# Optimization experiments

Measured on AMD Instinct MI355X. Metric: run time of the kernel, lower is better.

Reference implementation:

```python
import jax, jax.numpy as jnp
import numpy as np

N_NODES = 50000
N_EDGES = 800000
IN_FEATS = 256
HIDDEN = 128
HEADS = 2
NEG_SLOPE = 0.2


def gat_conv(x, edge_index, W, att_src, att_dst, bias, heads, out_c, concat):
    """PyG-style GATConv: linear -> per-edge attention logits -> segment
    softmax over destination neighborhoods -> scatter-add aggregate.
    Self-loops are added (PyG default add_self_loops=True)."""
    N = x.shape[0]
    h = (x @ W.T).reshape(N, heads, out_c)           # [N,H,C]
    loop = jnp.arange(N)
    src = jnp.concatenate([edge_index[0], loop])      # [E+N]
    dst = jnp.concatenate([edge_index[1], loop])
    a_src = jnp.sum(h * att_src, axis=-1)             # [N,H]
    a_dst = jnp.sum(h * att_dst, axis=-1)
    alpha = a_src[src] + a_dst[dst]                   # [E+N,H]
    alpha = jax.nn.leaky_relu(alpha, NEG_SLOPE)
    amax = jax.ops.segment_max(alpha, dst, num_segments=N)
    alpha = jnp.exp(alpha - amax[dst])
    denom = jax.ops.segment_sum(alpha, dst, num_segments=N)
    alpha = alpha / denom[dst]
    msg = h[src] * alpha[..., None]                   # [E+N,H,C]
    out = jax.ops.segment_sum(msg, dst, num_segments=N)  # [N,H,C]
    if concat:
        out = out.reshape(N, heads * out_c)
    else:
        out = out.mean(axis=1)
    return out + bias


def setup_inputs() -> dict:
    key = jax.random.key(0)
    ks = jax.random.split(key, 12)
    x = jax.random.normal(ks[0], (N_NODES, IN_FEATS), dtype=jnp.float32)
    edge_index = jax.random.randint(ks[1], (2, N_EDGES), 0, N_NODES, dtype=jnp.int64)
    s = 0.1
    W1 = jax.random.normal(ks[2], (HEADS * HIDDEN, IN_FEATS), dtype=jnp.float32) * s
    att_src1 = jax.random.normal(ks[3], (1, HEADS, HIDDEN), dtype=jnp.float32) * s
    att_dst1 = jax.random.normal(ks[4], (1, HEADS, HIDDEN), dtype=jnp.float32) * s
    b1 = jnp.zeros((HEADS * HIDDEN,), dtype=jnp.float32)
    W2 = jax.random.normal(ks[5], (HIDDEN, HEADS * HIDDEN), dtype=jnp.float32) * s
    att_src2 = jax.random.normal(ks[6], (1, 1, HIDDEN), dtype=jnp.float32) * s
    att_dst2 = jax.random.normal(ks[7], (1, 1, HIDDEN), dtype=jnp.float32) * s
    b2 = jnp.zeros((HIDDEN,), dtype=jnp.float32)
    return {"x": x, "edge_index": edge_index,
            "W1": W1, "att_src1": att_src1, "att_dst1": att_dst1, "b1": b1,
            "W2": W2, "att_src2": att_src2, "att_dst2": att_dst2, "b2": b2}


def reference(x, edge_index, W1, att_src1, att_dst1, b1, W2, att_src2, att_dst2, b2):
    h = gat_conv(x, edge_index, W1, att_src1, att_dst1, b1, HEADS, HIDDEN, True)
    h = jax.nn.relu(h)
    out = gat_conv(h, edge_index, W2, att_src2, att_dst2, b2, 1, HIDDEN, False)
    return out
```

## Files before the change

### kernel.cpp

```cpp
#include <hip/hip_runtime.h>
#include <hip/hip_bf16.h>


typedef _Float16 half8v __attribute__((ext_vector_type(8)));
typedef _Float16 half4v __attribute__((ext_vector_type(4)));
typedef _Float16 half2v __attribute__((ext_vector_type(2)));
typedef float f32x4 __attribute__((ext_vector_type(4)));


template <typename TA, int H, bool SCATTER>
__global__ __launch_bounds__(256) void gemm_att_kernel(
    const TA* __restrict__ A,
    const float* __restrict__ B,
    _Float16* __restrict__ C,
    const float* __restrict__ att_s,
    const float* __restrict__ att_d,
    float* __restrict__ a_s,
    float* __restrict__ a_d,
    int M, int K, int GB,
    const int* __restrict__ esrc, const int* __restrict__ edst,
    const int* __restrict__ rank, const int* __restrict__ csr_off,
    int* __restrict__ csr_src, int E, int nScatBlk)
{
    constexpr int BM = 128, BK = 32, LDA = 40;
    constexpr int NCOL = H * 128;
    __shared__ _Float16 Ah[BM * LDA];
    __shared__ _Float16 Bh[BM * LDA];
    __shared__ float red[2][2][64][2];

    const int tid = threadIdx.x;
    const int bid = blockIdx.x;

    if constexpr (SCATTER) {
        if (bid >= GB * H) {
            const int sbid = bid - GB * H;
            const int nq = (E + 3) >> 2;
            for (int q = sbid * 256 + tid; q < nq; q += nScatBlk * 256) {
                const int e4 = q * 4;
                if (e4 + 3 < E) {
                    const int4 sv = *reinterpret_cast<const int4*>(esrc + e4);
                    const int4 dv = *reinterpret_cast<const int4*>(edst + e4);
                    const int4 rv = *reinterpret_cast<const int4*>(rank + e4);
                    csr_src[csr_off[dv.x] + 1 + rv.x] = sv.x;
                    csr_src[csr_off[dv.y] + 1 + rv.y] = sv.y;
                    csr_src[csr_off[dv.z] + 1 + rv.z] = sv.z;
                    csr_src[csr_off[dv.w] + 1 + rv.w] = sv.w;
                } else {
                    for (int k = e4; k < E; ++k)
                        csr_src[csr_off[edst[k]] + 1 + rank[k]] = esrc[k];
                }
            }
            return;
        }
    }

    const int m0 = (bid % GB) * BM;
    const int by = bid / GB;
    const int n0 = by * 128;
    const int w  = tid >> 6;
    const int l  = tid & 63;
    const int wm = (w >> 1) * 64;
    const int wn = (w & 1) * 64;
    const int lr = l & 15;
    const int lq = l >> 4;

    f32x4 acc[4][4] = {};

    for (int k0 = 0; k0 < K; k0 += BK) {
        if constexpr (__is_same(TA, float)) {
#pragma unroll
            for (int it = 0; it < 4; ++it) {
                const int row = (tid >> 3) + it * 32;
                const int gm  = min(m0 + row, M - 1);
                const int c4  = (tid & 7) * 4;
                float4 v = *reinterpret_cast<const float4*>(A + (long)gm * K + k0 + c4);
                half4v o = { (_Float16)v.x, (_Float16)v.y, (_Float16)v.z, (_Float16)v.w };
                *reinterpret_cast<half4v*>(&Ah[row * LDA + c4]) = o;
            }
        } else {
#pragma unroll
            for (int it = 0; it < 2; ++it) {
                const int row = (tid >> 2) + it * 64;
                const int gm  = min(m0 + row, M - 1);
                const int c8  = (tid & 3) * 8;
                float4 v = *reinterpret_cast<const float4*>((const char*)A + ((long)gm * K + k0 + c8) * 2);
                *reinterpret_cast<float4*>(&Ah[row * LDA + c8]) = v;
            }
        }
#pragma unroll
        for (int it = 0; it < 4; ++it) {
            const int row = (tid >> 3) + it * 32;
            const int c4  = (tid & 7) * 4;
            float4 v = *reinterpret_cast<const float4*>(B + (long)(n0 + row) * K + k0 + c4);
            half4v o = { (_Float16)v.x, (_Float16)v.y, (_Float16)v.z, (_Float16)v.w };
            *reinterpret_cast<half4v*>(&Bh[row * LDA + c4]) = o;
        }
        __syncthreads();

        half8v af[4], bf[4];
#pragma unroll
        for (int i = 0; i < 4; ++i)
            af[i] = *reinterpret_cast<const half8v*>(&Ah[(wm + i * 16 + lr) * LDA + lq * 8]);
#pragma unroll
        for (int j = 0; j < 4; ++j)
            bf[j] = *reinterpret_cast<const half8v*>(&Bh[(wn + j * 16 + lr) * LDA + lq * 8]);
#pragma unroll
        for (int i = 0; i < 4; ++i)
#pragma unroll
            for (int j = 0; j < 4; ++j)
                acc[i][j] = __builtin_amdgcn_mfma_f32_16x16x32_f16(af[i], bf[j], acc[i][j], 0, 0, 0);
        __syncthreads();
    }

#pragma unroll
    for (int i = 0; i < 4; ++i) {
        const int gm_base = m0 + wm + i * 16 + lq * 4;
#pragma unroll
        for (int r = 0; r < 4; ++r) {
            const int gm = gm_base + r;
            if (gm < M) {
#pragma unroll
                for (int j = 0; j < 4; ++j)
                    C[(long)gm * NCOL + n0 + wn + j * 16 + lr] = (_Float16)acc[i][j][r];
            }
        }
    }

    float asv[4], adv[4];
#pragma unroll
    for (int j = 0; j < 4; ++j) {
        asv[j] = att_s[n0 + wn + j * 16 + lr];
        adv[j] = att_d[n0 + wn + j * 16 + lr];
    }
    float ps[4][4] = {}, pd[4][4] = {};
#pragma unroll
    for (int i = 0; i < 4; ++i)
#pragma unroll
        for (int j = 0; j < 4; ++j)
#pragma unroll
            for (int r = 0; r < 4; ++r) {
                ps[i][r] += acc[i][j][r] * asv[j];
                pd[i][r] += acc[i][j][r] * adv[j];
            }
#pragma unroll
    for (int o = 1; o < 16; o <<= 1)
#pragma unroll
        for (int i = 0; i < 4; ++i)
#pragma unroll
            for (int r = 0; r < 4; ++r) {
                ps[i][r] += __shfl_xor(ps[i][r], o, 64);
                pd[i][r] += __shfl_xor(pd[i][r], o, 64);
            }
    if (lr == 0) {
#pragma unroll
        for (int i = 0; i < 4; ++i)
#pragma unroll
            for (int r = 0; r < 4; ++r) {
                const int row = i * 16 + lq * 4 + r;
                red[wm >> 6][wn >> 6][row][0] = ps[i][r];
                red[wm >> 6][wn >> 6][row][1] = pd[i][r];
            }
    }
    __syncthreads();
    if (wn == 0) {
        const int row = l;
        const int gm = m0 + wm + row;
        if (gm < M) {
            const int wi = wm >> 6;
            a_s[(long)gm * H + by] = red[wi][0][row][0] + red[wi][1][row][0];
            a_d[(long)gm * H + by] = red[wi][0][row][1] + red[wi][1][row][1];
        }
    }
}


__global__ void count_kernel(const int* __restrict__ dst, int* __restrict__ deg,
                             int* __restrict__ rank, int E)
{
    const int tid = blockIdx.x * blockDim.x + threadIdx.x;
    const int e4 = tid * 4;
    if (e4 + 3 < E) {
        const int4 d = *reinterpret_cast<const int4*>(dst + e4);
        int4 r;
        r.x = atomicAdd(&deg[d.x], 1);
        r.y = atomicAdd(&deg[d.y], 1);
        r.z = atomicAdd(&deg[d.z], 1);
        r.w = atomicAdd(&deg[d.w], 1);
        *reinterpret_cast<int4*>(rank + e4) = r;
    } else if (e4 < E) {
        for (int k = e4; k < E; ++k) rank[k] = atomicAdd(&deg[dst[k]], 1);
    }
}

__global__ __launch_bounds__(256) void block_scan_kernel(
    const int* __restrict__ deg, int* __restrict__ pre, int* __restrict__ blk, int n)
{
    __shared__ int s[256];
    const int t = threadIdx.x;
    const int base = blockIdx.x * 1024 + t * 4;
    int4 d = make_int4(-1, -1, -1, -1);
    if (base + 3 < n) d = *reinterpret_cast<const int4*>(deg + base);
    else {
        if (base + 0 < n) d.x = deg[base + 0];
        if (base + 1 < n) d.y = deg[base + 1];
        if (base + 2 < n) d.z = deg[base + 2];
        if (base + 3 < n) d.w = deg[base + 3];
    }
    const int v0 = d.x + 1, v1 = d.y + 1, v2 = d.z + 1, v3 = d.w + 1;
    s[t] = v0 + v1 + v2 + v3;
    __syncthreads();
#pragma unroll
    for (int o = 1; o < 256; o <<= 1) {
        int val = 0;
        if (t >= o) val = s[t - o];
        __syncthreads();
        s[t] += val;
        __syncthreads();
    }
    int run = (t == 0) ? 0 : s[t - 1];
    int4 o4;
    o4.x = run; run += v0;
    o4.y = run; run += v1;
    o4.z = run; run += v2;
    o4.w = run; run += v3;
    if (base + 3 < n) *reinterpret_cast<int4*>(pre + base) = o4;
    else {
        if (base + 0 < n) pre[base + 0] = o4.x;
        if (base + 1 < n) pre[base + 1] = o4.y;
        if (base + 2 < n) pre[base + 2] = o4.z;
        if (base + 3 < n) pre[base + 3] = o4.w;
    }
    if (t == 255) blk[blockIdx.x] = s[255];
}

__global__ __launch_bounds__(256) void finalize_scan_kernel(
    const int* __restrict__ pre, const int* __restrict__ blk,
    int* __restrict__ off, int* __restrict__ csr_src, int n, int nvb)
{
    __shared__ int s_add;
    const int vb = blockIdx.x;
    const int t  = threadIdx.x;
    if (t < 64) {
        int v = (t < vb) ? blk[t] : 0;
#pragma unroll
        for (int o = 32; o > 0; o >>= 1) v += __shfl_xor(v, o, 64);
        if (t == 0) s_add = v;
    }
    __syncthreads();
    const int add = s_add;
    const int base = vb * 1024 + t * 4;
    if (base + 3 < n) {
        int4 p = *reinterpret_cast<const int4*>(pre + base);
        p.x += add; p.y += add; p.z += add; p.w += add;
        *reinterpret_cast<int4*>(off + base) = p;
        csr_src[p.x] = base + 0;
        csr_src[p.y] = base + 1;
        csr_src[p.z] = base + 2;
        csr_src[p.w] = base + 3;
    } else {
#pragma unroll
        for (int k = 0; k < 4; ++k)
            if (base + k < n) {
                const int v = pre[base + k] + add;
                off[base + k] = v;
                csr_src[v] = base + k;
            }
    }
    if (vb == nvb - 1 && t == 0) off[n] = add + blk[vb];
}


template <int H, int C, bool RELU, typename TOUT>
__global__ __launch_bounds__(256) void aggregate_kernel(
    const int* __restrict__ csr_off,
    const int* __restrict__ csr_src,
    const _Float16* __restrict__ h,
    const float* __restrict__ a_s,
    const float* __restrict__ a_d,
    const float* __restrict__ bias,
    TOUT* __restrict__ out,
    int N)
{
    constexpr int VPT = 8;
    constexpr int HC  = H * C;
    constexpr int LPE = HC / VPT;
    constexpr int GRP = 64 / LPE;

    const int w = threadIdx.x >> 6;
    const int l = threadIdx.x & 63;
    const int d = blockIdx.x * 4 + w;
    if (d >= N) return;

    const int g   = l / LPE;
    const int col = (l % LPE) * VPT;
    const int hh  = col / C;

    __shared__ float2 s_sw[4][64][H];

    const int beg = csr_off[d];
    const int end = csr_off[d + 1];

    float ad0 = 0.f, ad1 = 0.f;
    if constexpr (H == 2) {
        const float2 t2 = *reinterpret_cast<const float2*>(a_d + (long)d * 2);
        ad0 = t2.x; ad1 = t2.y;
    } else {
        ad0 = a_d[d];
    }

    float acc[VPT] = {};
    float wsum = 0.f;

    for (int base = beg; base < end; base += 64) {
        const int len  = min(64, end - base);
        const int lenp = (len + GRP - 1) & ~(GRP - 1);
        if (l < len) {
            const int s = csr_src[base + l];
            if constexpr (H == 2) {
                const float2 sv = *reinterpret_cast<const float2*>(a_s + (long)s * 2);
                float lg0 = sv.x + ad0; lg0 = lg0 > 0.f ? lg0 : 0.2f * lg0;
                float lg1 = sv.y + ad1; lg1 = lg1 > 0.f ? lg1 : 0.2f * lg1;
                s_sw[w][l][0] = make_float2(__int_as_float(s), __expf(lg0));
                s_sw[w][l][1] = make_float2(__int_as_float(s), __expf(lg1));
            } else {
                float lg = a_s[s] + ad0; lg = lg > 0.f ? lg : 0.2f * lg;
                s_sw[w][l][0] = make_float2(__int_as_float(s), __expf(lg));
            }
        } else if (l < lenp) {
#pragma unroll
            for (int h2 = 0; h2 < H; ++h2)
                s_sw[w][l][h2] = make_float2(__int_as_float(d), 0.f);
        }
        __builtin_amdgcn_wave_barrier();
#pragma unroll 2
        for (int jj = 0; jj < lenp; jj += GRP) {
            const float2 sw = s_sw[w][jj + g][hh];
            const int    s  = __float_as_int(sw.x);
            const float  wt = sw.y;
            const half8v hv = *reinterpret_cast<const half8v*>(
                h + (long)s * HC + col);
#pragma unroll
            for (int k = 0; k < VPT; ++k)
                acc[k] += wt * (float)hv[k];
            wsum += wt;
        }
        __builtin_amdgcn_wave_barrier();
    }

#pragma unroll
    for (int o = LPE; o < 64; o <<= 1) {
#pragma unroll
        for (int k = 0; k < VPT; ++k) acc[k] += __shfl_xor(acc[k], o, 64);
        wsum += __shfl_xor(wsum, o, 64);
    }

    if (g == 0) {
        const float inv = 1.f / wsum;
        float r[VPT];
#pragma unroll
        for (int k = 0; k < VPT; ++k) {
            r[k] = acc[k] * inv + bias[col + k];
            if (RELU) r[k] = r[k] > 0.f ? r[k] : 0.f;
        }
        if constexpr (__is_same(TOUT, _Float16)) {
            half8v ov;
#pragma unroll
            for (int k = 0; k < VPT; ++k) ov[k] = (_Float16)r[k];
            *reinterpret_cast<half8v*>(out + (long)d * HC + col) = ov;
        } else {
            f32x4 o0 = { r[0], r[1], r[2], r[3] };
            f32x4 o1 = { r[4], r[5], r[6], r[7] };
            *reinterpret_cast<f32x4*>(out + (long)d * HC + col)     = o0;
            *reinterpret_cast<f32x4*>(out + (long)d * HC + col + 4) = o1;
        }
    }
}


extern "C" void kernel_launch(void* const* d_in, const int* in_sizes, int n_in,
                              void* d_out, int out_size, void* d_ws, size_t ws_size,
                              hipStream_t stream)
{
    const float* x    = (const float*)d_in[0];
    const int*   eidx = (const int*)d_in[1];
    const float* W1   = (const float*)d_in[2];
    const float* as1  = (const float*)d_in[3];
    const float* ad1  = (const float*)d_in[4];
    const float* b1   = (const float*)d_in[5];
    const float* W2   = (const float*)d_in[6];
    const float* as2  = (const float*)d_in[7];
    const float* ad2  = (const float*)d_in[8];
    const float* b2   = (const float*)d_in[9];
    float* out = (float*)d_out;

    const int IN_FEATS = 256;
    const int N = in_sizes[0] / IN_FEATS;
    const int E = in_sizes[1] / 2;

    const int* esrc = eidx;
    const int* edst = eidx + E;

    size_t off = 0;
    auto alloc = [&](size_t bytes) -> void* {
        void* p = (char*)d_ws + off;
        off += (bytes + 255) & ~(size_t)255;
        return p;
    };
    _Float16* h1h   = (_Float16*)alloc((size_t)N * 256 * 2);
    _Float16* o1h   = (_Float16*)alloc((size_t)N * 256 * 2);
    _Float16* h2h   = (_Float16*)alloc((size_t)N * 128 * 2);
    float* a1s      = (float*)alloc((size_t)N * 2 * 4);
    float* a1d      = (float*)alloc((size_t)N * 2 * 4);
    float* a2s      = (float*)alloc((size_t)N * 4);
    float* a2d      = (float*)alloc((size_t)N * 4);
    int*   deg      = (int*)alloc((size_t)N * 4);
    int*   pre      = (int*)alloc((size_t)N * 4);
    int*   rank     = (int*)alloc((size_t)E * 4);
    int*   csr_off  = (int*)alloc((size_t)(N + 1) * 4);
    int*   csr_src  = (int*)alloc((size_t)(E + N) * 4);
    int*   blk      = (int*)alloc(64 * 4);

    const int nvb = (N + 1023) / 1024;

    hipMemsetAsync(deg, 0, (size_t)N * 4, stream);
    count_kernel<<<((E + 3) / 4 + 255) / 256, 256, 0, stream>>>(edst, deg, rank, E);
    block_scan_kernel<<<nvb, 256, 0, stream>>>(deg, pre, blk, N);
    finalize_scan_kernel<<<nvb, 256, 0, stream>>>(pre, blk, csr_off, csr_src, N, nvb);

    {
        const int GB = (N + 127) / 128;
        const int nScat = 192;
        gemm_att_kernel<float, 2, true><<<GB * 2 + nScat, 256, 0, stream>>>(
            x, W1, h1h, as1, ad1, a1s, a1d, N, 256, GB,
            esrc, edst, rank, csr_off, csr_src, E, nScat);
    }
    aggregate_kernel<2, 128, true, _Float16><<<(N + 3) / 4, 256, 0, stream>>>(
        csr_off, csr_src, h1h, a1s, a1d, b1, o1h, N);

    {
        const int GB = (N + 127) / 128;
        gemm_att_kernel<_Float16, 1, false><<<GB, 256, 0, stream>>>(
            o1h, W2, h2h, as2, ad2, a2s, a2d, N, 256, GB,
            nullptr, nullptr, nullptr, nullptr, nullptr, 0, 0);
    }
    aggregate_kernel<1, 128, false, float><<<(N + 3) / 4, 256, 0, stream>>>(
        csr_off, csr_src, h2h, a2s, a2d, b2, out, N);
}
```

Measured before the change: 292.7 us.

## Store features in 32-column sliced layout and aggregate per slice for cache locality

The GEMM outputs and first-layer aggregate outputs now use a column-sliced layout (32 fp16 columns per slice, each slice stored contiguously over all nodes). The aggregation kernel becomes persistent and grid-strided, and each block handles one slice, so the gathered working set per slice is small enough to stay in L2/LLC. Block-to-tile mapping in the first GEMM is swizzled so the two column halves of neighbouring row tiles run together. The cost is redundant re-reading of CSR indices and attention logits for every slice (eight times for layer one), plus narrower 8-byte gathers.

```diff
diff --git a/kernel.cpp b/kernel.cpp
--- a/kernel.cpp
+++ b/kernel.cpp
@@ -54,8 +54,15 @@
         }
     }
 
-    const int m0 = (bid % GB) * BM;
-    const int by = bid / GB;
+    int m0, by;
+    if (H == 2 && (GB & 7) == 0) {
+        const int cc = bid >> 4, jj = bid & 15;
+        m0 = ((cc << 3) + (jj & 7)) * BM;
+        by = jj >> 3;
+    } else {
+        m0 = (bid % GB) * BM;
+        by = bid / GB;
+    }
     const int n0 = by * 128;
     const int w  = tid >> 6;
     const int l  = tid & 63;
@@ -83,7 +90,9 @@
                 const int row = (tid >> 2) + it * 64;
                 const int gm  = min(m0 + row, M - 1);
                 const int c8  = (tid & 3) * 8;
-                float4 v = *reinterpret_cast<const float4*>((const char*)A + ((long)gm * K + k0 + c8) * 2);
+                const _Float16* src = (const _Float16*)A +
+                    ((size_t)(k0 >> 5) * M + gm) * 32 + c8;
+                float4 v = *reinterpret_cast<const float4*>(src);
                 *reinterpret_cast<float4*>(&Ah[row * LDA + c8]) = v;
             }
         }
@@ -120,8 +129,11 @@
             const int gm = gm_base + r;
             if (gm < M) {
 #pragma unroll
-                for (int j = 0; j < 4; ++j)
-                    C[(long)gm * NCOL + n0 + wn + j * 16 + lr] = (_Float16)acc[i][j][r];
+                for (int j = 0; j < 4; ++j) {
+                    const int col = n0 + wn + j * 16 + lr;
+                    C[((size_t)(col >> 5) * M + gm) * 32 + (col & 31)] =
+                        (_Float16)acc[i][j][r];
+                }
             }
         }
     }
@@ -279,99 +291,85 @@
     const float* __restrict__ a_d,
     const float* __restrict__ bias,
     TOUT* __restrict__ out,
-    int N)
-{
-    constexpr int VPT = 8;
+    int N, int G8)
+{
     constexpr int HC  = H * C;
-    constexpr int LPE = HC / VPT;
-    constexpr int GRP = 64 / LPE;
-
-    const int w = threadIdx.x >> 6;
-    const int l = threadIdx.x & 63;
-    const int d = blockIdx.x * 4 + w;
-    if (d >= N) return;
-
-    const int g   = l / LPE;
-    const int col = (l % LPE) * VPT;
-    const int hh  = col / C;
-
-    __shared__ float2 s_sw[4][64][H];
-
-    const int beg = csr_off[d];
-    const int end = csr_off[d + 1];
-
-    float ad0 = 0.f, ad1 = 0.f;
-    if constexpr (H == 2) {
-        const float2 t2 = *reinterpret_cast<const float2*>(a_d + (long)d * 2);
-        ad0 = t2.x; ad1 = t2.y;
-    } else {
-        ad0 = a_d[d];
-    }
-
-    float acc[VPT] = {};
-    float wsum = 0.f;
-
-    for (int base = beg; base < end; base += 64) {
-        const int len  = min(64, end - base);
-        const int lenp = (len + GRP - 1) & ~(GRP - 1);
-        if (l < len) {
-            const int s = csr_src[base + l];
-            if constexpr (H == 2) {
-                const float2 sv = *reinterpret_cast<const float2*>(a_s + (long)s * 2);
-                float lg0 = sv.x + ad0; lg0 = lg0 > 0.f ? lg0 : 0.2f * lg0;
-                float lg1 = sv.y + ad1; lg1 = lg1 > 0.f ? lg1 : 0.2f * lg1;
-                s_sw[w][l][0] = make_float2(__int_as_float(s), __expf(lg0));
-                s_sw[w][l][1] = make_float2(__int_as_float(s), __expf(lg1));
+    constexpr int NS  = HC / 32;
+    constexpr int REP = 8 / NS;
+    const int w  = threadIdx.x >> 6;
+    const int l  = threadIdx.x & 63;
+    const int b8 = blockIdx.x & 7;
+    const int slice = b8 % NS;
+    const int hh = (slice * 32) / C;
+    const int g2 = (blockIdx.x >> 3) * REP + b8 / NS;
+    const int dstride = G8 * REP * 4;
+    const int g  = l >> 3;
+    const int cl = (l & 7) * 4;
+
+    __shared__ float2 s_sw[4][64];
+    const _Float16* __restrict__ hs = h + (size_t)slice * N * 32;
+
+    for (int d = g2 * 4 + w; d < N; d += dstride) {
+        const int beg = csr_off[d];
+        const int end = csr_off[d + 1];
+        const float ad = a_d[d * H + hh];
+        float acc[4] = {};
+        float wsum = 0.f;
+
+        for (int base = beg; base < end; base += 64) {
+            const int len = min(64, end - base);
+            float2 sw;
+            if (l < len) {
+                const int s = __builtin_nontemporal_load(csr_src + base + l);
+                float lg = a_s[s * H + hh] + ad;
+                lg = lg > 0.f ? lg : 0.2f * lg;
+                sw = make_float2(__int_as_float(s), __expf(lg));
             } else {
-                float lg = a_s[s] + ad0; lg = lg > 0.f ? lg : 0.2f * lg;
-                s_sw[w][l][0] = make_float2(__int_as_float(s), __expf(lg));
-            }
-        } else if (l < lenp) {
-#pragma unroll
-            for (int h2 = 0; h2 < H; ++h2)
-                s_sw[w][l][h2] = make_float2(__int_as_float(d), 0.f);
-        }
-        __builtin_amdgcn_wave_barrier();
-#pragma unroll 2
-        for (int jj = 0; jj < lenp; jj += GRP) {
-            const float2 sw = s_sw[w][jj + g][hh];
-            const int    s  = __float_as_int(sw.x);
-            const float  wt = sw.y;
-            const half8v hv = *reinterpret_cast<const half8v*>(
-                h + (long)s * HC + col);
-#pragma unroll
-            for (int k = 0; k < VPT; ++k)
-                acc[k] += wt * (float)hv[k];
-            wsum += wt;
-        }
-        __builtin_amdgcn_wave_barrier();
-    }
-
-#pragma unroll
-    for (int o = LPE; o < 64; o <<= 1) {
-#pragma unroll
-        for (int k = 0; k < VPT; ++k) acc[k] += __shfl_xor(acc[k], o, 64);
-        wsum += __shfl_xor(wsum, o, 64);
-    }
-
-    if (g == 0) {
-        const float inv = 1.f / wsum;
-        float r[VPT];
-#pragma unroll
-        for (int k = 0; k < VPT; ++k) {
-            r[k] = acc[k] * inv + bias[col + k];
-            if (RELU) r[k] = r[k] > 0.f ? r[k] : 0.f;
-        }
-        if constexpr (__is_same(TOUT, _Float16)) {
-            half8v ov;
-#pragma unroll
-            for (int k = 0; k < VPT; ++k) ov[k] = (_Float16)r[k];
-            *reinterpret_cast<half8v*>(out + (long)d * HC + col) = ov;
-        } else {
-            f32x4 o0 = { r[0], r[1], r[2], r[3] };
-            f32x4 o1 = { r[4], r[5], r[6], r[7] };
-            *reinterpret_cast<f32x4*>(out + (long)d * HC + col)     = o0;
-            *reinterpret_cast<f32x4*>(out + (long)d * HC + col + 4) = o1;
+                sw = make_float2(__int_as_float(d), 0.f);
+            }
+            s_sw[w][l] = sw;
+            __builtin_amdgcn_wave_barrier();
+            const int iters = (len + 7) >> 3;
+            for (int jj = 0; jj < iters; ++jj) {
+                const float2 e = s_sw[w][jj * 8 + g];
+                const int    s = __float_as_int(e.x);
+                const float wt = e.y;
+                const half4v hv = *reinterpret_cast<const half4v*>(
+                    hs + (size_t)s * 32 + cl);
+                acc[0] += wt * (float)hv.x;
+                acc[1] += wt * (float)hv.y;
+                acc[2] += wt * (float)hv.z;
+                acc[3] += wt * (float)hv.w;
+                wsum += wt;
+            }
+            __builtin_amdgcn_wave_barrier();
+        }
+
+#pragma unroll
+        for (int o = 8; o < 64; o <<= 1) {
+#pragma unroll
+            for (int k = 0; k < 4; ++k) acc[k] += __shfl_xor(acc[k], o, 64);
+            wsum += __shfl_xor(wsum, o, 64);
+        }
+
+        if (g == 0) {
+            const float inv = 1.f / wsum;
+            float r[4];
+#pragma unroll
+            for (int k = 0; k < 4; ++k) {
+                r[k] = acc[k] * inv + bias[slice * 32 + cl + k];
+                if (RELU) r[k] = r[k] > 0.f ? r[k] : 0.f;
+            }
+            if constexpr (__is_same(TOUT, _Float16)) {
+                half4v ov = { (_Float16)r[0], (_Float16)r[1],
+                              (_Float16)r[2], (_Float16)r[3] };
+                *reinterpret_cast<half4v*>(
+                    out + ((size_t)slice * N + d) * 32 + cl) = ov;
+            } else {
+                f32x4 ov = { r[0], r[1], r[2], r[3] };
+                *reinterpret_cast<f32x4*>(
+                    out + (size_t)d * HC + slice * 32 + cl) = ov;
+            }
         }
     }
 }
@@ -434,8 +432,11 @@
             x, W1, h1h, as1, ad1, a1s, a1d, N, 256, GB,
             esrc, edst, rank, csr_off, csr_src, E, nScat);
     }
-    aggregate_kernel<2, 128, true, _Float16><<<(N + 3) / 4, 256, 0, stream>>>(
-        csr_off, csr_src, h1h, a1s, a1d, b1, o1h, N);
+    {
+        const int G8 = 256;
+        aggregate_kernel<2, 128, true, _Float16><<<G8 * 8, 256, 0, stream>>>(
+            csr_off, csr_src, h1h, a1s, a1d, b1, o1h, N, G8);
+    }
 
     {
         const int GB = (N + 127) / 128;
@@ -443,6 +444,9 @@
             o1h, W2, h2h, as2, ad2, a2s, a2d, N, 256, GB,
             nullptr, nullptr, nullptr, nullptr, nullptr, 0, 0);
     }
-    aggregate_kernel<1, 128, false, float><<<(N + 3) / 4, 256, 0, stream>>>(
-        csr_off, csr_src, h2h, a2s, a2d, b2, out, N);
-}
+    {
+        const int G8 = 256;
+        aggregate_kernel<1, 128, false, float><<<G8 * 8, 256, 0, stream>>>(
+            csr_off, csr_src, h2h, a2s, a2d, b2, out, N, G8);
+    }
+}
```

New measurement: 435.1 us. 48.7% more time.
